# Kernel optimization log

Hardware: AMD Instinct MI355X
Metric: run time of the kernel (lower is better)

The kernel has to match this reference:

```python
import jax, jax.numpy as jnp
import numpy as np

ITERATIONS = 3

def setup_inputs() -> dict:
    key = jax.random.key(0)
    k1, k2 = jax.random.split(key)
    C, S, H = 64, 128, 2048
    x = jax.random.normal(k1, (C, S, H), dtype=jnp.float32)
    W = jax.random.normal(k2, (H, H), dtype=jnp.float32)
    return {"x": x, "W": W}

def reference(x, W):
    # x: [C, S, H], W: [H, H]
    C, S, H = x.shape
    # e_ij is loop-invariant in the original; hoist it (same math, computed once)
    e_ij = jnp.einsum('csh,hk->csk', x, W)  # [C, S, H]
    b_ij = jnp.zeros((C, S), dtype=x.dtype)
    c_i = jnp.zeros((C, H), dtype=x.dtype)
    for _ in range(ITERATIONS):
        d_i = jax.nn.softmax(b_ij, axis=1)[:, :, None]          # [C, S, 1], softmax over S
        c_i = jnp.sum(d_i * e_ij, axis=1)                        # [C, H]
        squared = jnp.sum(c_i ** 2, axis=1, keepdims=True)       # [C, 1]
        coeff = squared / (1.0 + squared) / jnp.sqrt(squared + 1e-9)
        c_i = coeff * c_i                                        # squash
        b_ij = b_ij + jnp.einsum('csh,ch->cs', e_ij, c_i)        # logit update
    return c_i
```

## Files before the change

### kernel.cpp

```cpp
#include <hip/hip_runtime.h>

using bf16x8 = __attribute__((ext_vector_type(8))) __bf16;
using f32x4  = __attribute__((ext_vector_type(4))) float;

#define C_ 64
#define S_ 128
#define H_ 2048
#define M_ 8192

__device__ __forceinline__ unsigned short f2bf(float f) {
  unsigned u = __float_as_uint(f);
  u = u + 0x7fffu + ((u >> 16) & 1u);
  return (unsigned short)(u >> 16);
}
__device__ __forceinline__ float bf2f(unsigned short h) {
  return __uint_as_float(((unsigned)h) << 16);
}

__device__ __forceinline__ void glds16(const unsigned short* g, unsigned short* l) {
  __builtin_amdgcn_global_load_lds(
      (const __attribute__((address_space(1))) void*)g,
      (__attribute__((address_space(3))) void*)l, 16, 0, 0);
}

__global__ void k_split_all(const float* __restrict__ x,
                            unsigned short* __restrict__ xh,
                            unsigned short* __restrict__ xl,
                            const float* __restrict__ W,
                            unsigned short* __restrict__ Wth,
                            unsigned short* __restrict__ Wtl,
                            float* __restrict__ G) {
  __shared__ float Ts[64][68];
  const int b = blockIdx.x;
  const int t = threadIdx.x;
  if (b < 16384) {
    int idx = b * 256 + t;
    float4 v = ((const float4*)x)[idx];
    float a[4] = {v.x, v.y, v.z, v.w};
    unsigned short h[4], l[4];
#pragma unroll
    for (int q = 0; q < 4; ++q) {
      h[q] = f2bf(a[q]);
      l[q] = f2bf(a[q] - bf2f(h[q]));
    }
    ((ushort4*)xh)[idx] = make_ushort4(h[0], h[1], h[2], h[3]);
    ((ushort4*)xl)[idx] = make_ushort4(l[0], l[1], l[2], l[3]);
  } else if (b < 17408) {
    const int bb = b - 16384;
    const int k0 = (bb & 31) * 64, n0 = (bb >> 5) * 64;
#pragma unroll
    for (int p = 0; p < 4; ++p) {
      int idx = t + p * 256;
      int r = idx >> 4, c4 = (idx & 15) * 4;
      *(float4*)&Ts[r][c4] = *(const float4*)(W + (size_t)(k0 + r) * H_ + n0 + c4);
    }
    __syncthreads();
#pragma unroll
    for (int p = 0; p < 4; ++p) {
      int idx = t + p * 256;
      int rr = idx >> 4, cc = (idx & 15) * 4;
      unsigned short h[4], l[4];
#pragma unroll
      for (int q = 0; q < 4; ++q) {
        float f = Ts[cc + q][rr];
        h[q] = f2bf(f);
        l[q] = f2bf(f - bf2f(h[q]));
      }
      size_t o = (size_t)(n0 + rr) * H_ + k0 + cc;
      *(ushort4*)(Wth + o) = make_ushort4(h[0], h[1], h[2], h[3]);
      *(ushort4*)(Wtl + o) = make_ushort4(l[0], l[1], l[2], l[3]);
    }
  } else {
    const int bb = b - 17408;
    ((float4*)G)[bb * 256 + t] = (float4){0.f, 0.f, 0.f, 0.f};
  }
}

__global__ __launch_bounds__(256, 4) void k_gemm3(
    const unsigned short* __restrict__ Ah, const unsigned short* __restrict__ Al,
    const unsigned short* __restrict__ Bh, const unsigned short* __restrict__ Bl,
    unsigned short* __restrict__ Eh, unsigned short* __restrict__ El) {
  __shared__ unsigned short sAh[128 * 32], sAl[128 * 32], sBh[128 * 32], sBl[128 * 32];
  const int t = threadIdx.x;
  const int bn = blockIdx.x, bm = blockIdx.y;
  const int lane = t & 63, wid = t >> 6;
  const int wm = wid >> 1, wn = wid & 1;
  const int l16 = lane & 15, quad = lane >> 4;

  const int rl = lane >> 2;
  const int gg = (lane & 3) ^ ((rl >> 1) & 3);
  const int c0 = wid * 2, c1 = wid * 2 + 1;
  const unsigned short* gAh0 = Ah + (size_t)(bm * 128 + c0 * 16 + rl) * H_ + gg * 8;
  const unsigned short* gAh1 = Ah + (size_t)(bm * 128 + c1 * 16 + rl) * H_ + gg * 8;
  const unsigned short* gAl0 = Al + (size_t)(bm * 128 + c0 * 16 + rl) * H_ + gg * 8;
  const unsigned short* gAl1 = Al + (size_t)(bm * 128 + c1 * 16 + rl) * H_ + gg * 8;
  const unsigned short* gBh0 = Bh + (size_t)(bn * 128 + c0 * 16 + rl) * H_ + gg * 8;
  const unsigned short* gBh1 = Bh + (size_t)(bn * 128 + c1 * 16 + rl) * H_ + gg * 8;
  const unsigned short* gBl0 = Bl + (size_t)(bn * 128 + c0 * 16 + rl) * H_ + gg * 8;
  const unsigned short* gBl1 = Bl + (size_t)(bn * 128 + c1 * 16 + rl) * H_ + gg * 8;
  unsigned short* lA0 = sAh + c0 * 512;
  unsigned short* lA1 = sAh + c1 * 512;
  unsigned short* lAl0 = sAl + c0 * 512;
  unsigned short* lAl1 = sAl + c1 * 512;
  unsigned short* lB0 = sBh + c0 * 512;
  unsigned short* lB1 = sBh + c1 * 512;
  unsigned short* lBl0 = sBl + c0 * 512;
  unsigned short* lBl1 = sBl + c1 * 512;

  const int swz = ((l16 >> 1) & 3);
  const int colq = ((quad ^ swz) * 8);

  f32x4 acc[4][4];
#pragma unroll
  for (int i = 0; i < 4; ++i)
#pragma unroll
    for (int j = 0; j < 4; ++j) acc[i][j] = (f32x4)0.f;

  for (int k0 = 0; k0 < H_; k0 += 32) {
    __syncthreads();
    glds16(gAh0 + k0, lA0);
    glds16(gAh1 + k0, lA1);
    glds16(gAl0 + k0, lAl0);
    glds16(gAl1 + k0, lAl1);
    glds16(gBh0 + k0, lB0);
    glds16(gBh1 + k0, lB1);
    glds16(gBl0 + k0, lBl0);
    glds16(gBl1 + k0, lBl1);
    __syncthreads();

    bf16x8 ah[4], al[4], bh[4], bl[4];
#pragma unroll
    for (int i = 0; i < 4; ++i) {
      const int ra = (wm * 64 + i * 16 + l16) * 32;
      const int rb = (wn * 64 + i * 16 + l16) * 32;
      ah[i] = *(const bf16x8*)&sAh[ra + colq];
      al[i] = *(const bf16x8*)&sAl[ra + colq];
      bh[i] = *(const bf16x8*)&sBh[rb + colq];
      bl[i] = *(const bf16x8*)&sBl[rb + colq];
    }
#pragma unroll
    for (int i = 0; i < 4; ++i)
#pragma unroll
      for (int j = 0; j < 4; ++j) {
        acc[i][j] = __builtin_amdgcn_mfma_f32_16x16x32_bf16(ah[i], bh[j], acc[i][j], 0, 0, 0);
        acc[i][j] = __builtin_amdgcn_mfma_f32_16x16x32_bf16(ah[i], bl[j], acc[i][j], 0, 0, 0);
        acc[i][j] = __builtin_amdgcn_mfma_f32_16x16x32_bf16(al[i], bh[j], acc[i][j], 0, 0, 0);
      }
  }

#pragma unroll
  for (int i = 0; i < 4; ++i) {
    const int row0 = bm * 128 + wm * 64 + i * 16 + quad * 4;
#pragma unroll
    for (int j = 0; j < 4; ++j) {
      const int col = bn * 128 + wn * 64 + j * 16 + l16;
#pragma unroll
      for (int r = 0; r < 4; ++r) {
        float v = acc[i][j][r];
        unsigned short hh = f2bf(v);
        unsigned short ll = f2bf(v - bf2f(hh));
        Eh[(size_t)(row0 + r) * H_ + col] = hh;
        El[(size_t)(row0 + r) * H_ + col] = ll;
      }
    }
  }
}

__global__ __launch_bounds__(256, 4) void k_gram_mfma(
    const unsigned short* __restrict__ Eh, const unsigned short* __restrict__ El,
    float* __restrict__ G) {
  __shared__ unsigned short sH[128 * 32], sL[128 * 32];
  const int t = threadIdx.x;
  const int kc = blockIdx.x;
  const int cc = blockIdx.y;
  const int lane = t & 63, wid = t >> 6;
  const int wm = wid >> 1, wn = wid & 1;
  const int l16 = lane & 15, quad = lane >> 4;

  const int rl = lane >> 2;
  const int gg = (lane & 3) ^ ((rl >> 1) & 3);
  const int c0 = wid * 2, c1 = c0 + 1;
  const size_t kbase = (size_t)kc * 256 + gg * 8;
  const unsigned short* gH0 = Eh + (size_t)(cc * 128 + c0 * 16 + rl) * H_ + kbase;
  const unsigned short* gH1 = Eh + (size_t)(cc * 128 + c1 * 16 + rl) * H_ + kbase;
  const unsigned short* gL0 = El + (size_t)(cc * 128 + c0 * 16 + rl) * H_ + kbase;
  const unsigned short* gL1 = El + (size_t)(cc * 128 + c1 * 16 + rl) * H_ + kbase;
  unsigned short* lH0 = sH + c0 * 512;
  unsigned short* lH1 = sH + c1 * 512;
  unsigned short* lL0 = sL + c0 * 512;
  unsigned short* lL1 = sL + c1 * 512;

  const int swz = ((l16 >> 1) & 3);
  const int colq = ((quad ^ swz) * 8);

  f32x4 acc[4][4];
#pragma unroll
  for (int i = 0; i < 4; ++i)
#pragma unroll
    for (int j = 0; j < 4; ++j) acc[i][j] = (f32x4)0.f;

  for (int k0 = 0; k0 < 256; k0 += 32) {
    __syncthreads();
    glds16(gH0 + k0, lH0);
    glds16(gH1 + k0, lH1);
    glds16(gL0 + k0, lL0);
    glds16(gL1 + k0, lL1);
    __syncthreads();

    bf16x8 ah[4], al[4], bh[4], bl[4];
#pragma unroll
    for (int i = 0; i < 4; ++i) {
      const int ra = (wm * 64 + i * 16 + l16) * 32;
      const int rb = (wn * 64 + i * 16 + l16) * 32;
      ah[i] = *(const bf16x8*)&sH[ra + colq];
      al[i] = *(const bf16x8*)&sL[ra + colq];
      bh[i] = *(const bf16x8*)&sH[rb + colq];
      bl[i] = *(const bf16x8*)&sL[rb + colq];
    }
#pragma unroll
    for (int i = 0; i < 4; ++i)
#pragma unroll
      for (int j = 0; j < 4; ++j) {
        acc[i][j] = __builtin_amdgcn_mfma_f32_16x16x32_bf16(ah[i], bh[j], acc[i][j], 0, 0, 0);
        acc[i][j] = __builtin_amdgcn_mfma_f32_16x16x32_bf16(ah[i], bl[j], acc[i][j], 0, 0, 0);
        acc[i][j] = __builtin_amdgcn_mfma_f32_16x16x32_bf16(al[i], bh[j], acc[i][j], 0, 0, 0);
      }
  }

  float* Gc = G + (size_t)cc * S_ * S_;
#pragma unroll
  for (int i = 0; i < 4; ++i) {
    const int row0 = wm * 64 + i * 16 + quad * 4;
#pragma unroll
    for (int j = 0; j < 4; ++j) {
      const int col = wn * 64 + j * 16 + l16;
#pragma unroll
      for (int r = 0; r < 4; ++r)
        atomicAdd(&Gc[(row0 + r) * S_ + col], acc[i][j][r]);
    }
  }
}

__global__ void k_out2(const unsigned short* __restrict__ Eh,
                       const unsigned short* __restrict__ El,
                       const float* __restrict__ G, float* __restrict__ out) {
  const int c = blockIdx.y;
  const int s = threadIdx.x & 127;
  __shared__ float dsh[128];
  __shared__ float red[128];
  __shared__ float wsh[128];
  const float* Gc = G + (size_t)c * S_ * S_;
  float b = 0.f;
  for (int it = 0; it < 3; ++it) {
    red[s] = b; __syncthreads();
    for (int off = 64; off > 0; off >>= 1) {
      if (s < off) red[s] = fmaxf(red[s], red[s + off]);
      __syncthreads();
    }
    float mx = red[0]; __syncthreads();
    float ev = expf(b - mx);
    red[s] = ev; __syncthreads();
    for (int off = 64; off > 0; off >>= 1) {
      if (s < off) red[s] = red[s] + red[s + off];
      __syncthreads();
    }
    float Z = red[0]; __syncthreads();
    float d = ev / Z;
    dsh[s] = d; __syncthreads();
    float y = 0.f;
#pragma unroll 8
    for (int j = 0; j < S_; ++j) y = fmaf(Gc[j * S_ + s], dsh[j], y);
    red[s] = d * y; __syncthreads();
    for (int off = 64; off > 0; off >>= 1) {
      if (s < off) red[s] = red[s] + red[s + off];
      __syncthreads();
    }
    float sq = red[0]; __syncthreads();
    float coeff = sq / (1.f + sq) / sqrtf(sq + 1e-9f);
    if (it == 2) wsh[s] = coeff * d;
    else b += coeff * y;
  }
  __syncthreads();

  const int h2 = blockIdx.x * 256 + threadIdx.x;
  const unsigned* Ph = (const unsigned*)(Eh + (size_t)c * S_ * H_) + h2;
  const unsigned* Pl = (const unsigned*)(El + (size_t)c * S_ * H_) + h2;
  float a0 = 0.f, a1 = 0.f;
#pragma unroll 8
  for (int ss = 0; ss < S_; ++ss) {
    unsigned uh = Ph[(size_t)ss * (H_ / 2)];
    unsigned ul = Pl[(size_t)ss * (H_ / 2)];
    a0 = fmaf(wsh[ss], bf2f((unsigned short)uh) + bf2f((unsigned short)ul), a0);
    a1 = fmaf(wsh[ss], bf2f((unsigned short)(uh >> 16)) + bf2f((unsigned short)(ul >> 16)), a1);
  }
  ((float2*)(out + (size_t)c * H_))[h2] = make_float2(a0, a1);
}

extern "C" void kernel_launch(void* const* d_in, const int* in_sizes, int n_in,
                              void* d_out, int out_size, void* d_ws, size_t ws_size,
                              hipStream_t stream) {
  (void)in_sizes; (void)n_in; (void)out_size; (void)ws_size;
  const float* x = (const float*)d_in[0];
  const float* W = (const float*)d_in[1];
  float* out = (float*)d_out;
  char* ws = (char*)d_ws;

  unsigned short* xh  = (unsigned short*)(ws);
  unsigned short* xl  = (unsigned short*)(ws + 33554432);
  unsigned short* Wth = (unsigned short*)(ws + 67108864);
  unsigned short* Wtl = (unsigned short*)(ws + 75497472);
  unsigned short* Eh  = (unsigned short*)(ws + 83886080);
  unsigned short* El  = (unsigned short*)(ws + 117440512);
  float*          G   = (float*)(ws + 150994944);

  k_split_all<<<dim3(18432), 256, 0, stream>>>(x, xh, xl, W, Wth, Wtl, G);
  k_gemm3<<<dim3(16, 64), 256, 0, stream>>>(xh, xl, Wth, Wtl, Eh, El);
  k_gram_mfma<<<dim3(8, 64), 256, 0, stream>>>(Eh, El, G);
  k_out2<<<dim3(4, 64), 256, 0, stream>>>(Eh, El, G, out);
}
```

Baseline: 380.5 us.

## Warp-specialize GEMM with producer waves and double-buffered LDS

Block size grows to 384 threads. Two extra waves act as producers, issuing global-to-LDS loads for the next K slice into a double buffer, while the four MFMA waves compute on the current slice. This aims to overlap memory latency with the split-bf16 MFMA work instead of loading and computing in serialized phases. It doubles LDS use, which can lower occupancy, and one barrier per iteration still couples the producer and consumer waves.

```diff
diff --git a/kernel.cpp b/kernel.cpp
--- a/kernel.cpp
+++ b/kernel.cpp
@@ -76,37 +76,26 @@
   }
 }
 
-__global__ __launch_bounds__(256, 4) void k_gemm3(
+__global__ __launch_bounds__(384, 3) void k_gemm3(
     const unsigned short* __restrict__ Ah, const unsigned short* __restrict__ Al,
     const unsigned short* __restrict__ Bh, const unsigned short* __restrict__ Bl,
     unsigned short* __restrict__ Eh, unsigned short* __restrict__ El) {
-  __shared__ unsigned short sAh[128 * 32], sAl[128 * 32], sBh[128 * 32], sBl[128 * 32];
+  __shared__ unsigned short sAh[2 * 4096], sAl[2 * 4096], sBh[2 * 4096], sBl[2 * 4096];
   const int t = threadIdx.x;
   const int bn = blockIdx.x, bm = blockIdx.y;
   const int lane = t & 63, wid = t >> 6;
+
+  const int rl = lane >> 2;
+  const int gg = (lane & 3) ^ ((rl >> 1) & 3);
+
+  const unsigned short* pAh = Ah + (size_t)(bm * 128 + rl) * H_ + gg * 8;
+  const unsigned short* pAl = Al + (size_t)(bm * 128 + rl) * H_ + gg * 8;
+  const unsigned short* pBh = Bh + (size_t)(bn * 128 + rl) * H_ + gg * 8;
+  const unsigned short* pBl = Bl + (size_t)(bn * 128 + rl) * H_ + gg * 8;
+  const int pid = wid - 4;
+
   const int wm = wid >> 1, wn = wid & 1;
   const int l16 = lane & 15, quad = lane >> 4;
-
-  const int rl = lane >> 2;
-  const int gg = (lane & 3) ^ ((rl >> 1) & 3);
-  const int c0 = wid * 2, c1 = wid * 2 + 1;
-  const unsigned short* gAh0 = Ah + (size_t)(bm * 128 + c0 * 16 + rl) * H_ + gg * 8;
-  const unsigned short* gAh1 = Ah + (size_t)(bm * 128 + c1 * 16 + rl) * H_ + gg * 8;
-  const unsigned short* gAl0 = Al + (size_t)(bm * 128 + c0 * 16 + rl) * H_ + gg * 8;
-  const unsigned short* gAl1 = Al + (size_t)(bm * 128 + c1 * 16 + rl) * H_ + gg * 8;
-  const unsigned short* gBh0 = Bh + (size_t)(bn * 128 + c0 * 16 + rl) * H_ + gg * 8;
-  const unsigned short* gBh1 = Bh + (size_t)(bn * 128 + c1 * 16 + rl) * H_ + gg * 8;
-  const unsigned short* gBl0 = Bl + (size_t)(bn * 128 + c0 * 16 + rl) * H_ + gg * 8;
-  const unsigned short* gBl1 = Bl + (size_t)(bn * 128 + c1 * 16 + rl) * H_ + gg * 8;
-  unsigned short* lA0 = sAh + c0 * 512;
-  unsigned short* lA1 = sAh + c1 * 512;
-  unsigned short* lAl0 = sAl + c0 * 512;
-  unsigned short* lAl1 = sAl + c1 * 512;
-  unsigned short* lB0 = sBh + c0 * 512;
-  unsigned short* lB1 = sBh + c1 * 512;
-  unsigned short* lBl0 = sBl + c0 * 512;
-  unsigned short* lBl1 = sBl + c1 * 512;
-
   const int swz = ((l16 >> 1) & 3);
   const int colq = ((quad ^ swz) * 8);
 
@@ -116,51 +105,71 @@
 #pragma unroll
     for (int j = 0; j < 4; ++j) acc[i][j] = (f32x4)0.f;
 
-  for (int k0 = 0; k0 < H_; k0 += 32) {
+  if (wid >= 4) {
+#pragma unroll
+    for (int c = 0; c < 4; ++c) {
+      const int ch = pid * 4 + c;
+      const size_t go = (size_t)(ch * 16) * H_;
+      glds16(pAh + go, sAh + ch * 512);
+      glds16(pAl + go, sAl + ch * 512);
+      glds16(pBh + go, sBh + ch * 512);
+      glds16(pBl + go, sBl + ch * 512);
+    }
+  }
+  __syncthreads();
+
+  for (int k0 = 0; k0 < 64; ++k0) {
+    if (wid < 4) {
+      const int bo = (k0 & 1) * 4096;
+      bf16x8 ah[4], al[4], bh[4], bl[4];
+#pragma unroll
+      for (int i = 0; i < 4; ++i) {
+        const int ra = bo + (wm * 64 + i * 16 + l16) * 32;
+        const int rb = bo + (wn * 64 + i * 16 + l16) * 32;
+        ah[i] = *(const bf16x8*)&sAh[ra + colq];
+        al[i] = *(const bf16x8*)&sAl[ra + colq];
+        bh[i] = *(const bf16x8*)&sBh[rb + colq];
+        bl[i] = *(const bf16x8*)&sBl[rb + colq];
+      }
+#pragma unroll
+      for (int i = 0; i < 4; ++i)
+#pragma unroll
+        for (int j = 0; j < 4; ++j) {
+          acc[i][j] = __builtin_amdgcn_mfma_f32_16x16x32_bf16(ah[i], bh[j], acc[i][j], 0, 0, 0);
+          acc[i][j] = __builtin_amdgcn_mfma_f32_16x16x32_bf16(ah[i], bl[j], acc[i][j], 0, 0, 0);
+          acc[i][j] = __builtin_amdgcn_mfma_f32_16x16x32_bf16(al[i], bh[j], acc[i][j], 0, 0, 0);
+        }
+    } else if (k0 + 1 < 64) {
+      const int nb = ((k0 + 1) & 1) * 4096;
+      const int kk = (k0 + 1) * 32;
+#pragma unroll
+      for (int c = 0; c < 4; ++c) {
+        const int ch = pid * 4 + c;
+        const size_t go = (size_t)(ch * 16) * H_ + kk;
+        glds16(pAh + go, sAh + nb + ch * 512);
+        glds16(pAl + go, sAl + nb + ch * 512);
+        glds16(pBh + go, sBh + nb + ch * 512);
+        glds16(pBl + go, sBl + nb + ch * 512);
+      }
+    }
     __syncthreads();
-    glds16(gAh0 + k0, lA0);
-    glds16(gAh1 + k0, lA1);
-    glds16(gAl0 + k0, lAl0);
-    glds16(gAl1 + k0, lAl1);
-    glds16(gBh0 + k0, lB0);
-    glds16(gBh1 + k0, lB1);
-    glds16(gBl0 + k0, lBl0);
-    glds16(gBl1 + k0, lBl1);
-    __syncthreads();
-
-    bf16x8 ah[4], al[4], bh[4], bl[4];
+  }
+
+  if (wid < 4) {
 #pragma unroll
     for (int i = 0; i < 4; ++i) {
-      const int ra = (wm * 64 + i * 16 + l16) * 32;
-      const int rb = (wn * 64 + i * 16 + l16) * 32;
-      ah[i] = *(const bf16x8*)&sAh[ra + colq];
-      al[i] = *(const bf16x8*)&sAl[ra + colq];
-      bh[i] = *(const bf16x8*)&sBh[rb + colq];
-      bl[i] = *(const bf16x8*)&sBl[rb + colq];
-    }
-#pragma unroll
-    for (int i = 0; i < 4; ++i)
+      const int row0 = bm * 128 + wm * 64 + i * 16 + quad * 4;
 #pragma unroll
       for (int j = 0; j < 4; ++j) {
-        acc[i][j] = __builtin_amdgcn_mfma_f32_16x16x32_bf16(ah[i], bh[j], acc[i][j], 0, 0, 0);
-        acc[i][j] = __builtin_amdgcn_mfma_f32_16x16x32_bf16(ah[i], bl[j], acc[i][j], 0, 0, 0);
-        acc[i][j] = __builtin_amdgcn_mfma_f32_16x16x32_bf16(al[i], bh[j], acc[i][j], 0, 0, 0);
-      }
-  }
-
-#pragma unroll
-  for (int i = 0; i < 4; ++i) {
-    const int row0 = bm * 128 + wm * 64 + i * 16 + quad * 4;
-#pragma unroll
-    for (int j = 0; j < 4; ++j) {
-      const int col = bn * 128 + wn * 64 + j * 16 + l16;
-#pragma unroll
-      for (int r = 0; r < 4; ++r) {
-        float v = acc[i][j][r];
-        unsigned short hh = f2bf(v);
-        unsigned short ll = f2bf(v - bf2f(hh));
-        Eh[(size_t)(row0 + r) * H_ + col] = hh;
-        El[(size_t)(row0 + r) * H_ + col] = ll;
+        const int col = bn * 128 + wn * 64 + j * 16 + l16;
+#pragma unroll
+        for (int r = 0; r < 4; ++r) {
+          float v = acc[i][j][r];
+          unsigned short hh = f2bf(v);
+          unsigned short ll = f2bf(v - bf2f(hh));
+          Eh[(size_t)(row0 + r) * H_ + col] = hh;
+          El[(size_t)(row0 + r) * H_ + col] = ll;
+        }
       }
     }
   }
@@ -314,7 +323,7 @@
   float*          G   = (float*)(ws + 150994944);
 
   k_split_all<<<dim3(18432), 256, 0, stream>>>(x, xh, xl, W, Wth, Wtl, G);
-  k_gemm3<<<dim3(16, 64), 256, 0, stream>>>(xh, xl, Wth, Wtl, Eh, El);
+  k_gemm3<<<dim3(16, 64), 384, 0, stream>>>(xh, xl, Wth, Wtl, Eh, El);
   k_gram_mfma<<<dim3(8, 64), 256, 0, stream>>>(Eh, El, G);
   k_out2<<<dim3(4, 64), 256, 0, stream>>>(Eh, El, G, out);
 }
```

Measured after the change: 388.7 us. 2.1% more time.

## Load A fragments directly from global and double-buffer B tile in LDS

Applied to the files above, without the earlier changes.

The GEMM kernel no longer stages the A operand (hi/lo bf16 split) in shared memory. Each wave now reads its A fragments straight from global memory into registers, while the B tile is double-buffered in LDS so the next k-slice's async loads overlap the current MFMAs, with one barrier per iteration instead of two. This removes LDS traffic and a sync per step. In exchange, each A tile is read from global/L2 by both wn waves without reuse through LDS, and the direct loads bring register pressure and global-latency exposure.

```diff
diff --git a/kernel.cpp b/kernel.cpp
--- a/kernel.cpp
+++ b/kernel.cpp
@@ -80,7 +80,7 @@
     const unsigned short* __restrict__ Ah, const unsigned short* __restrict__ Al,
     const unsigned short* __restrict__ Bh, const unsigned short* __restrict__ Bl,
     unsigned short* __restrict__ Eh, unsigned short* __restrict__ El) {
-  __shared__ unsigned short sAh[128 * 32], sAl[128 * 32], sBh[128 * 32], sBl[128 * 32];
+  __shared__ unsigned short sBh[2 * 4096], sBl[2 * 4096];
   const int t = threadIdx.x;
   const int bn = blockIdx.x, bm = blockIdx.y;
   const int lane = t & 63, wid = t >> 6;
@@ -90,22 +90,19 @@
   const int rl = lane >> 2;
   const int gg = (lane & 3) ^ ((rl >> 1) & 3);
   const int c0 = wid * 2, c1 = wid * 2 + 1;
-  const unsigned short* gAh0 = Ah + (size_t)(bm * 128 + c0 * 16 + rl) * H_ + gg * 8;
-  const unsigned short* gAh1 = Ah + (size_t)(bm * 128 + c1 * 16 + rl) * H_ + gg * 8;
-  const unsigned short* gAl0 = Al + (size_t)(bm * 128 + c0 * 16 + rl) * H_ + gg * 8;
-  const unsigned short* gAl1 = Al + (size_t)(bm * 128 + c1 * 16 + rl) * H_ + gg * 8;
   const unsigned short* gBh0 = Bh + (size_t)(bn * 128 + c0 * 16 + rl) * H_ + gg * 8;
   const unsigned short* gBh1 = Bh + (size_t)(bn * 128 + c1 * 16 + rl) * H_ + gg * 8;
   const unsigned short* gBl0 = Bl + (size_t)(bn * 128 + c0 * 16 + rl) * H_ + gg * 8;
   const unsigned short* gBl1 = Bl + (size_t)(bn * 128 + c1 * 16 + rl) * H_ + gg * 8;
-  unsigned short* lA0 = sAh + c0 * 512;
-  unsigned short* lA1 = sAh + c1 * 512;
-  unsigned short* lAl0 = sAl + c0 * 512;
-  unsigned short* lAl1 = sAl + c1 * 512;
-  unsigned short* lB0 = sBh + c0 * 512;
-  unsigned short* lB1 = sBh + c1 * 512;
-  unsigned short* lBl0 = sBl + c0 * 512;
-  unsigned short* lBl1 = sBl + c1 * 512;
+
+  const unsigned short* gA_h[4];
+  const unsigned short* gA_l[4];
+#pragma unroll
+  for (int i = 0; i < 4; ++i) {
+    const size_t ro = (size_t)(bm * 128 + wm * 64 + i * 16 + l16) * H_ + quad * 8;
+    gA_h[i] = Ah + ro;
+    gA_l[i] = Al + ro;
+  }
 
   const int swz = ((l16 >> 1) & 3);
   const int colq = ((quad ^ swz) * 8);
@@ -116,36 +113,45 @@
 #pragma unroll
     for (int j = 0; j < 4; ++j) acc[i][j] = (f32x4)0.f;
 
-  for (int k0 = 0; k0 < H_; k0 += 32) {
+  glds16(gBh0, sBh + c0 * 512);
+  glds16(gBh1, sBh + c1 * 512);
+  glds16(gBl0, sBl + c0 * 512);
+  glds16(gBl1, sBl + c1 * 512);
+  __syncthreads();
+
+  for (int k0 = 0; k0 < 64; ++k0) {
+    const int bo = (k0 & 1) * 4096;
+    const int kk = k0 * 32;
+
+    bf16x8 ah[4], al[4];
+#pragma unroll
+    for (int i = 0; i < 4; ++i) {
+      ah[i] = *(const bf16x8*)(gA_h[i] + kk);
+      al[i] = *(const bf16x8*)(gA_l[i] + kk);
+    }
+
+    if (k0 + 1 < 64) {
+      const int nb = 4096 - bo;
+      const int kn = kk + 32;
+      glds16(gBh0 + kn, sBh + nb + c0 * 512);
+      glds16(gBh1 + kn, sBh + nb + c1 * 512);
+      glds16(gBl0 + kn, sBl + nb + c0 * 512);
+      glds16(gBl1 + kn, sBl + nb + c1 * 512);
+    }
+
+#pragma unroll
+    for (int j = 0; j < 4; ++j) {
+      const int rb = bo + (wn * 64 + j * 16 + l16) * 32;
+      bf16x8 bh = *(const bf16x8*)&sBh[rb + colq];
+      bf16x8 bl = *(const bf16x8*)&sBl[rb + colq];
+#pragma unroll
+      for (int i = 0; i < 4; ++i) {
+        acc[i][j] = __builtin_amdgcn_mfma_f32_16x16x32_bf16(ah[i], bh, acc[i][j], 0, 0, 0);
+        acc[i][j] = __builtin_amdgcn_mfma_f32_16x16x32_bf16(ah[i], bl, acc[i][j], 0, 0, 0);
+        acc[i][j] = __builtin_amdgcn_mfma_f32_16x16x32_bf16(al[i], bh, acc[i][j], 0, 0, 0);
+      }
+    }
     __syncthreads();
-    glds16(gAh0 + k0, lA0);
-    glds16(gAh1 + k0, lA1);
-    glds16(gAl0 + k0, lAl0);
-    glds16(gAl1 + k0, lAl1);
-    glds16(gBh0 + k0, lB0);
-    glds16(gBh1 + k0, lB1);
-    glds16(gBl0 + k0, lBl0);
-    glds16(gBl1 + k0, lBl1);
-    __syncthreads();
-
-    bf16x8 ah[4], al[4], bh[4], bl[4];
-#pragma unroll
-    for (int i = 0; i < 4; ++i) {
-      const int ra = (wm * 64 + i * 16 + l16) * 32;
-      const int rb = (wn * 64 + i * 16 + l16) * 32;
-      ah[i] = *(const bf16x8*)&sAh[ra + colq];
-      al[i] = *(const bf16x8*)&sAl[ra + colq];
-      bh[i] = *(const bf16x8*)&sBh[rb + colq];
-      bl[i] = *(const bf16x8*)&sBl[rb + colq];
-    }
-#pragma unroll
-    for (int i = 0; i < 4; ++i)
-#pragma unroll
-      for (int j = 0; j < 4; ++j) {
-        acc[i][j] = __builtin_amdgcn_mfma_f32_16x16x32_bf16(ah[i], bh[j], acc[i][j], 0, 0, 0);
-        acc[i][j] = __builtin_amdgcn_mfma_f32_16x16x32_bf16(ah[i], bl[j], acc[i][j], 0, 0, 0);
-        acc[i][j] = __builtin_amdgcn_mfma_f32_16x16x32_bf16(al[i], bh[j], acc[i][j], 0, 0, 0);
-      }
   }
 
 #pragma unroll
```

New measurement: 489.7 us. 1.29x slower.
